# Optimization experiments

Hardware: AMD Instinct MI355X
Metric: run time of the kernel (lower is better)

Reference implementation:

```python
import jax, jax.numpy as jnp
import numpy as np

B = 8
DIM = 256          # __init__ dim; input has 2*DIM channels
H = 32
W = 32
NUM_HEADS = 4
DH_QK = 64         # make_divisible(256*1.0, 8) // 4
DH_V = 64          # dim_out // num_heads
DQK = NUM_HEADS * DH_QK   # 256
DV = NUM_HEADS * DH_V     # 256
SCALE = DH_QK ** -0.5
HIDDEN = 4 * DIM          # mlp_ratio=4 applied to dim
DIM_OUT = DIM
EPS = 1e-5


def setup_inputs() -> dict:
    key = jax.random.key(0)
    ks = jax.random.split(key, 8)
    qkv_out = 2 * DQK + DV   # 768
    return {
        "x": jax.random.normal(ks[0], (B, 2 * DIM, H, W), jnp.float32),
        "qkv_f_w": jax.random.normal(ks[1], (qkv_out, DIM), jnp.float32) * DIM ** -0.5,
        "qkv_p_w": jax.random.normal(ks[2], (qkv_out, DIM), jnp.float32) * DIM ** -0.5,
        "height_rel": jax.random.normal(ks[3], (2 * H - 1, DH_QK), jnp.float32) * SCALE,
        "width_rel": jax.random.normal(ks[4], (2 * W - 1, DH_QK), jnp.float32) * SCALE,
        "ln_gamma": jnp.ones((2 * DV, H, W), jnp.float32),
        "ln_beta": jnp.zeros((2 * DV, H, W), jnp.float32),
        "fc1_w": jax.random.normal(ks[5], (HIDDEN, 2 * DV), jnp.float32) * (2 * DV) ** -0.5,
        "fc1_b": jnp.zeros((HIDDEN,), jnp.float32),
        "fc2_w": jax.random.normal(ks[6], (DIM_OUT, HIDDEN), jnp.float32) * HIDDEN ** -0.5,
        "fc2_b": jnp.zeros((DIM_OUT,), jnp.float32),
    }


def _rel_to_abs(x):
    # x: (b, L, 2L-1) -> (b, L, L) via the pad/reshape shift trick
    b, L, _ = x.shape
    x = jnp.pad(x, ((0, 0), (0, 0), (0, 1)))          # (b, L, 2L)
    xf = x.reshape(b, L * 2 * L)
    xf = jnp.pad(xf, ((0, 0), (0, L - 1)))
    return xf.reshape(b, L + 1, 2 * L - 1)[:, :L, L - 1:]


def _rel_logits_1d(q, rel_k, perm):
    # q: (b, h, w, d); rel_k: (2w-1, d) -> (b, h, w, h, w) after perm
    b, h, w, _ = q.shape
    x = jnp.einsum('bhwd,md->bhwm', q, rel_k).reshape(b * h, w, 2 * w - 1)
    x = _rel_to_abs(x).reshape(b, h, 1, w, w)
    x = jnp.broadcast_to(x, (b, h, h, w, w))
    return x.transpose(perm)


def _pos_embed(q, height_rel, width_rel):
    # q: (B*nh, HW, d) -> relative-position logits (B*nh, HW, HW)
    bh = q.shape[0]
    qs = q.reshape(bh, H, W, DH_QK)
    lw = _rel_logits_1d(qs, width_rel, (0, 1, 3, 2, 4))
    lh = _rel_logits_1d(qs.transpose(0, 2, 1, 3), height_rel, (0, 3, 1, 4, 2))
    return (lh + lw).reshape(bh, H * W, H * W)


def _get_qkv(x, w):
    # 1x1 conv as channel GEMM; x: (B, DIM, H, W)
    qkv = jnp.einsum('bchw,oc->bohw', x, w)
    q, k, v = jnp.split(qkv, [DQK, 2 * DQK], axis=1)
    q = q.reshape(B * NUM_HEADS, DH_QK, H * W).transpose(0, 2, 1)  # (Bh, HW, d)
    k = k.reshape(B * NUM_HEADS, DH_QK, H * W)                      # (Bh, d, HW)
    v = v.reshape(B * NUM_HEADS, DH_V, H * W).transpose(0, 2, 1)    # (Bh, HW, d)
    return q, k, v


def _apply_attn(q, k, v, height_rel, width_rel):
    logits = jnp.einsum('bnd,bdm->bnm', q, k) * SCALE + _pos_embed(q, height_rel, width_rel)
    attn = jax.nn.softmax(logits, axis=-1)
    out = jnp.einsum('bnm,bmd->bnd', attn, v)                       # (Bh, HW, dv)
    return out.transpose(0, 2, 1).reshape(B, DV, H, W)


def reference(x, qkv_f_w, qkv_p_w, height_rel, width_rel, ln_gamma, ln_beta,
              fc1_w, fc1_b, fc2_w, fc2_b):
    x1, x2 = x[:, :DIM], x[:, DIM:]
    qf, kf, vf = _get_qkv(x1, qkv_f_w)
    qp, kp, vp = _get_qkv(x2, qkv_p_w)
    out_f = _apply_attn(qf, kp, vp, height_rel, width_rel)
    out_p = _apply_attn(qp, kf, vf, height_rel, width_rel)
    xpf = jnp.concatenate([out_f, out_p], axis=1)                   # (B, 2*DV, H, W)
    # LayerNorm over normalized_shape = [2*DV, H, W]
    mean = xpf.mean(axis=(1, 2, 3), keepdims=True)
    var = jnp.var(xpf, axis=(1, 2, 3), keepdims=True)
    xpf = (xpf - mean) * jax.lax.rsqrt(var + EPS) * ln_gamma + ln_beta
    # conv-MLP (1x1 convs), exact GELU as torch default
    h = jnp.einsum('bchw,oc->bohw', xpf, fc1_w) + fc1_b[None, :, None, None]
    h = jax.nn.gelu(h, approximate=False)
    out = jnp.einsum('bchw,oc->bohw', h, fc2_w) + fc2_b[None, :, None, None]
    return out  # stride=1 -> pool is identity
```

## Files before the change

kernel.cpp:

```cpp
#include <hip/hip_runtime.h>

#define SCALE 0.125f

typedef short short8 __attribute__((ext_vector_type(8)));
typedef float f32x4 __attribute__((ext_vector_type(4)));
typedef unsigned short us8 __attribute__((ext_vector_type(8)));

typedef __attribute__((address_space(1))) const void gvoid;
typedef __attribute__((address_space(3))) void svoid;
__device__ __forceinline__ void gll16(const void* g, void* l) {
  __builtin_amdgcn_global_load_lds((gvoid*)g, (svoid*)l, 16, 0, 0);
}

__device__ __forceinline__ unsigned short f2bf(float x) {
  unsigned int u = __float_as_uint(x);
  u += 0x7fff + ((u >> 16) & 1);
  return (unsigned short)(u >> 16);
}
__device__ __forceinline__ float bf2f(unsigned short b) {
  return __uint_as_float(((unsigned int)b) << 16);
}
__device__ __forceinline__ float gelu_exact(float x) {
  return 0.5f * x * (1.0f + erff(x * 0.70710678118654752f));
}

__global__ __launch_bounds__(256)
void cast_w(const float* __restrict__ qf, const float* __restrict__ qp,
            const float* __restrict__ f1, const float* __restrict__ f2,
            unsigned short* __restrict__ wc)
{
  const int i4 = (blockIdx.x * 256 + threadIdx.x) * 4;
  const float* src; int off;
  if (i4 < 196608)      { src = qf; off = i4; }
  else if (i4 < 393216) { src = qp; off = i4 - 196608; }
  else if (i4 < 917504) { src = f1; off = i4 - 393216; }
  else                  { src = f2; off = i4 - 917504; }
  const float4 v = *(const float4*)(src + off);
  ushort4 o;
  o.x = f2bf(v.x); o.y = f2bf(v.y); o.z = f2bf(v.z); o.w = f2bf(v.w);
  *(ushort4*)(wc + i4) = o;
}

__global__ __launch_bounds__(256)
void trans_x(const float* __restrict__ x, unsigned short* __restrict__ xT)
{
  __shared__ unsigned short L[64 * 72];
  const int ch0 = blockIdx.x * 64, tok0 = blockIdx.y * 64, z = blockIdx.z;
  const int b = z & 7, path = z >> 3;
  const float* src = x + (size_t)b * 524288 + (size_t)(path * 256 + ch0) * 1024 + tok0;
#pragma unroll
  for (int t = 0; t < 4; ++t) {
    const int i = threadIdx.x + t * 256;
    const int row = i >> 4, c4 = (i & 15) * 4;
    const float4 v = *(const float4*)(src + (size_t)row * 1024 + c4);
    L[(c4 + 0) * 72 + row] = f2bf(v.x);
    L[(c4 + 1) * 72 + row] = f2bf(v.y);
    L[(c4 + 2) * 72 + row] = f2bf(v.z);
    L[(c4 + 3) * 72 + row] = f2bf(v.w);
  }
  __syncthreads();
  unsigned short* dst = xT + (size_t)z * 262144 + (size_t)tok0 * 256 + ch0;
#pragma unroll
  for (int t = 0; t < 2; ++t) {
    const int i = threadIdx.x + t * 256;
    const int row = i >> 3, c8 = (i & 7) * 8;
    *(us8*)(dst + (size_t)row * 256 + c8) = *(const us8*)&L[row * 72 + c8];
  }
}

__global__ __launch_bounds__(256)
void trans_gb(const float* __restrict__ gamma, const float* __restrict__ beta,
              unsigned short* __restrict__ gbT)
{
  __shared__ unsigned short L[64 * 72];
  const int ch0 = blockIdx.x * 64, tok0 = blockIdx.y * 64, which = blockIdx.z;
  const float* src = (which ? beta : gamma) + (size_t)ch0 * 1024 + tok0;
#pragma unroll
  for (int t = 0; t < 4; ++t) {
    const int i = threadIdx.x + t * 256;
    const int row = i >> 4, c4 = (i & 15) * 4;
    const float4 v = *(const float4*)(src + (size_t)row * 1024 + c4);
    L[(c4 + 0) * 72 + row] = f2bf(v.x);
    L[(c4 + 1) * 72 + row] = f2bf(v.y);
    L[(c4 + 2) * 72 + row] = f2bf(v.z);
    L[(c4 + 3) * 72 + row] = f2bf(v.w);
  }
  __syncthreads();
  unsigned short* dst = gbT + (size_t)which * 524288 + (size_t)tok0 * 512 + ch0;
#pragma unroll
  for (int t = 0; t < 2; ++t) {
    const int i = threadIdx.x + t * 256;
    const int row = i >> 3, c8 = (i & 7) * 8;
    *(us8*)(dst + (size_t)row * 512 + c8) = *(const us8*)&L[row * 72 + c8];
  }
}

template<int MODE, int LD, int KLEN>
__global__ __launch_bounds__(256, 3)
void gemm_mf(const unsigned short* __restrict__ A0, const unsigned short* __restrict__ B0,
             unsigned short* __restrict__ qkT, unsigned short* __restrict__ vb,
             unsigned short* __restrict__ hT, float* __restrict__ outF,
             const float* __restrict__ bias)
{
  __shared__ unsigned short As[2][4096];
  __shared__ unsigned short Bs[2][4096];
  const int tid = threadIdx.x;
  const int lane = tid & 63, w = tid >> 6;
  const int c = lane & 15, g = lane >> 4;
  const int wm = w >> 1, wn = w & 1;
  const int m0 = blockIdx.x * 128, n0 = blockIdx.y * 128;
  const int z = blockIdx.z;

  const unsigned short* A;
  const unsigned short* B;
  int zb = z, kc = 0;
  if (MODE == 0) {
    A = A0 + (size_t)(z >> 3) * 196608;
    B = B0 + (size_t)z * 262144;
  } else if (MODE == 1) {
    A = A0;
    B = B0 + (size_t)z * 1024 * LD;
  } else {
    zb = z >> 1; kc = z & 1;
    A = A0 + kc * KLEN;
    B = B0 + (size_t)zb * 1024 * LD + kc * KLEN;
  }

  f32x4 acc[4][4];
#pragma unroll
  for (int mi = 0; mi < 4; ++mi)
#pragma unroll
    for (int ni = 0; ni < 4; ++ni) acc[mi][ni] = (f32x4){0.f, 0.f, 0.f, 0.f};

  const int srow = tid >> 2;
  const int skc8 = (tid & 3) * 8;
  const int sbase = (tid & 192) * 8;

#pragma unroll
  for (int t = 0; t < 2; ++t) {
    gll16(A + (size_t)(m0 + srow + t * 64) * LD + skc8, &As[0][sbase + t * 2048]);
    gll16(B + (size_t)(n0 + srow + t * 64) * LD + skc8, &Bs[0][sbase + t * 2048]);
  }

  const int NK = KLEN / 32;
  for (int ks = 0; ks < NK; ++ks) {
    __syncthreads();
    if (ks + 1 < NK) {
      const int k0 = (ks + 1) * 32;
      const int nb = (ks + 1) & 1;
#pragma unroll
      for (int t = 0; t < 2; ++t) {
        gll16(A + (size_t)(m0 + srow + t * 64) * LD + k0 + skc8, &As[nb][sbase + t * 2048]);
        gll16(B + (size_t)(n0 + srow + t * 64) * LD + k0 + skc8, &Bs[nb][sbase + t * 2048]);
      }
    }
    const unsigned short* Asb = As[ks & 1];
    const unsigned short* Bsb = Bs[ks & 1];
    short8 aF[4], bF[4];
#pragma unroll
    for (int mi = 0; mi < 4; ++mi)
      aF[mi] = *(const short8*)&Asb[(64 * wm + 16 * mi + c) * 32 + g * 8];
#pragma unroll
    for (int ni = 0; ni < 4; ++ni)
      bF[ni] = *(const short8*)&Bsb[(64 * wn + 16 * ni + c) * 32 + g * 8];
#pragma unroll
    for (int mi = 0; mi < 4; ++mi)
#pragma unroll
      for (int ni = 0; ni < 4; ++ni)
        acc[mi][ni] = __builtin_amdgcn_mfma_f32_16x16x32_bf16(aF[mi], bF[ni], acc[mi][ni], 0, 0, 0);
  }

  if (MODE == 0) {
#pragma unroll
    for (int mi = 0; mi < 4; ++mi) {
      const int mb = m0 + 64 * wm + 16 * mi + 4 * g;
#pragma unroll
      for (int ni = 0; ni < 4; ++ni) {
        const int n = n0 + 64 * wn + 16 * ni + c;
        if (mb < 512) {
          ushort4 o4;
          o4.x = f2bf(acc[mi][ni][0]); o4.y = f2bf(acc[mi][ni][1]);
          o4.z = f2bf(acc[mi][ni][2]); o4.w = f2bf(acc[mi][ni][3]);
          *(ushort4*)(qkT + (size_t)z * 524288 + (size_t)n * 512 + mb) = o4;
        } else {
#pragma unroll
          for (int r = 0; r < 4; ++r)
            vb[(size_t)z * 262144 + (size_t)(mb - 512 + r) * 1024 + n] = f2bf(acc[mi][ni][r]);
        }
      }
    }
  } else if (MODE == 1) {
#pragma unroll
    for (int mi = 0; mi < 4; ++mi) {
      const int mb = m0 + 64 * wm + 16 * mi + 4 * g;
      const float4 b4 = *(const float4*)(bias + mb);
#pragma unroll
      for (int ni = 0; ni < 4; ++ni) {
        const int n = n0 + 64 * wn + 16 * ni + c;
        ushort4 o4;
        o4.x = f2bf(gelu_exact(acc[mi][ni][0] + b4.x));
        o4.y = f2bf(gelu_exact(acc[mi][ni][1] + b4.y));
        o4.z = f2bf(gelu_exact(acc[mi][ni][2] + b4.z));
        o4.w = f2bf(gelu_exact(acc[mi][ni][3] + b4.w));
        *(ushort4*)(hT + (size_t)z * 1048576 + (size_t)n * 1024 + mb) = o4;
      }
    }
  } else {
#pragma unroll
    for (int mi = 0; mi < 4; ++mi) {
      const int mb = m0 + 64 * wm + 16 * mi + 4 * g;
      float4 b4 = make_float4(0.f, 0.f, 0.f, 0.f);
      if (kc == 0) b4 = *(const float4*)(bias + mb);
#pragma unroll
      for (int ni = 0; ni < 4; ++ni) {
        const int n = n0 + 64 * wn + 16 * ni + c;
        float* op = outF + (size_t)zb * 262144 + (size_t)mb * 1024 + n;
        atomicAdd(&op[0],    acc[mi][ni][0] + b4.x);
        atomicAdd(&op[1024], acc[mi][ni][1] + b4.y);
        atomicAdd(&op[2048], acc[mi][ni][2] + b4.z);
        atomicAdd(&op[3072], acc[mi][ni][3] + b4.w);
      }
    }
  }
}

__global__ __launch_bounds__(256, 2)
void attn_k(const unsigned short* __restrict__ qkT,
            const unsigned short* __restrict__ vbuf,
            const float* __restrict__ hrel,
            const float* __restrict__ wrel,
            unsigned short* __restrict__ xpfT,
            float* __restrict__ stats)
{
  __shared__ unsigned short Kb[2][4096];
  __shared__ unsigned short Vb[2][4096];
  __shared__ unsigned short Ps[128 * 72];
  __shared__ unsigned short QHt[128 * 34];

  const int tid = threadIdx.x;
  const int lane = tid & 63, w = tid >> 6;
  const int c = lane & 15, g = lane >> 4;
  const int xb = blockIdx.x;
  const int pOut = xb >> 5, bh = xb & 31;
  const int b = bh >> 2, head = bh & 3, pKV = 1 - pOut;
  const int n0 = blockIdx.y * 128;
  const int rb = 32 * w;

  const unsigned short* Qg = qkT + (size_t)(pOut * 8 + b) * 524288 + head * 64;
  const unsigned short* Kg = qkT + (size_t)(pKV * 8 + b) * 524288 + 256 + head * 64;
  const unsigned short* Vg = vbuf + ((size_t)(pKV * 8 + b) * 256 + head * 64) * 1024;

  us8 kr[2], vr[2];
#pragma unroll
  for (int t = 0; t < 2; ++t) {
    const int i = tid + t * 256;
    const int row = i >> 3, ch = i & 7;
    kr[t] = *(const us8*)(Kg + (size_t)row * 512 + ch * 8);
    vr[t] = *(const us8*)(Vg + (size_t)row * 1024 + ch * 8);
  }

  short8 bQ[2][2];
#pragma unroll
  for (int grp = 0; grp < 2; ++grp) {
    const unsigned short* qp = Qg + (size_t)(n0 + rb + 16 * grp + c) * 512 + 8 * g;
    bQ[grp][0] = *(const short8*)(qp);
    bQ[grp][1] = *(const short8*)(qp + 32);
  }

#pragma unroll
  for (int f = 0; f < 4; ++f) {
    const int rr = 16 * f + c;
    const int rrc = rr < 63 ? rr : 62;
    const float sc = rr < 63 ? 1.f : 0.f;
    short8 w0, w1, h0, h1;
#pragma unroll
    for (int j = 0; j < 8; ++j) {
      w0[j] = f2bf(wrel[rrc * 64 + 8 * g + j] * sc);
      w1[j] = f2bf(wrel[rrc * 64 + 32 + 8 * g + j] * sc);
      h0[j] = f2bf(hrel[rrc * 64 + 8 * g + j] * sc);
      h1[j] = f2bf(hrel[rrc * 64 + 32 + 8 * g + j] * sc);
    }
#pragma unroll
    for (int grp = 0; grp < 2; ++grp) {
      f32x4 zw = {0.f, 0.f, 0.f, 0.f};
      zw = __builtin_amdgcn_mfma_f32_16x16x32_bf16(w0, bQ[grp][0], zw, 0, 0, 0);
      zw = __builtin_amdgcn_mfma_f32_16x16x32_bf16(w1, bQ[grp][1], zw, 0, 0, 0);
      f32x4 zh = {0.f, 0.f, 0.f, 0.f};
      zh = __builtin_amdgcn_mfma_f32_16x16x32_bf16(h0, bQ[grp][0], zh, 0, 0, 0);
      zh = __builtin_amdgcn_mfma_f32_16x16x32_bf16(h1, bQ[grp][1], zh, 0, 0, 0);
      const int qrow = rb + 16 * grp + c;
      ushort4 pw;
      pw.x = f2bf(zw[0]); pw.y = f2bf(zw[1]); pw.z = f2bf(zw[2]); pw.w = f2bf(zw[3]);
      *(ushort4*)&Ps[qrow * 72 + 16 * f + 4 * g] = pw;
      const int h1i = (n0 + qrow) >> 5;
#pragma unroll
      for (int r = 0; r < 4; ++r) {
        const int h2 = 16 * f + 4 * g + r - 31 + h1i;
        if (h2 >= 0 && h2 < 32) QHt[qrow * 34 + h2] = f2bf(zh[r]);
      }
    }
  }

  float qwv[2][2][4];
#pragma unroll
  for (int grp = 0; grp < 2; ++grp) {
    const int qrow = rb + 16 * grp + c;
    const int w1i = (n0 + qrow) & 31;
#pragma unroll
    for (int p = 0; p < 2; ++p)
#pragma unroll
      for (int r = 0; r < 4; ++r)
        qwv[grp][p][r] = bf2f(Ps[qrow * 72 + (16 * p + 4 * g + r - w1i + 31)]);
  }

#pragma unroll
  for (int t = 0; t < 2; ++t) {
    const int i = tid + t * 256;
    const int row = i >> 3, ch = i & 7;
    const int p = row * 64 + ((ch ^ (row & 7)) * 8);
    *(us8*)&Kb[0][p] = kr[t];
    *(us8*)&Vb[0][p] = vr[t];
  }

  float lsum[2] = {0.f, 0.f};
  f32x4 O[2][4];
#pragma unroll
  for (int grp = 0; grp < 2; ++grp)
#pragma unroll
    for (int f = 0; f < 4; ++f) O[grp][f] = (f32x4){0.f, 0.f, 0.f, 0.f};

  for (int mt = 0; mt < 16; ++mt) {
    __syncthreads();
    if (mt < 15) {
      const int m0n = (mt + 1) * 64;
#pragma unroll
      for (int t = 0; t < 2; ++t) {
        const int i = tid + t * 256;
        const int row = i >> 3, ch = i & 7;
        kr[t] = *(const us8*)(Kg + (size_t)(m0n + row) * 512 + ch * 8);
        vr[t] = *(const us8*)(Vg + (size_t)row * 1024 + m0n + ch * 8);
      }
    }
    const unsigned short* Ks = Kb[mt & 1];
    const unsigned short* Vs = Vb[mt & 1];

    short8 kA[4][2];
#pragma unroll
    for (int f = 0; f < 4; ++f) {
      const int row = 16 * f + c;
      kA[f][0] = *(const short8*)&Ks[row * 64 + ((g ^ (row & 7)) * 8)];
      kA[f][1] = *(const short8*)&Ks[row * 64 + (((4 + g) ^ (row & 7)) * 8)];
    }
#pragma unroll
    for (int grp = 0; grp < 2; ++grp) {
      const int qrow = rb + 16 * grp + c;
      const float qh0 = bf2f(QHt[qrow * 34 + 2 * mt]);
      const float qh1 = bf2f(QHt[qrow * 34 + 2 * mt + 1]);
#pragma unroll
      for (int f = 0; f < 4; ++f) {
        f32x4 z = {0.f, 0.f, 0.f, 0.f};
        z = __builtin_amdgcn_mfma_f32_16x16x32_bf16(kA[f][0], bQ[grp][0], z, 0, 0, 0);
        z = __builtin_amdgcn_mfma_f32_16x16x32_bf16(kA[f][1], bQ[grp][1], z, 0, 0, 0);
        const float qh = (f >= 2) ? qh1 : qh0;
        const float* qwp = qwv[grp][f & 1];
        const float p0 = __expf(fmaf(z[0], SCALE, qh + qwp[0]));
        const float p1 = __expf(fmaf(z[1], SCALE, qh + qwp[1]));
        const float p2 = __expf(fmaf(z[2], SCALE, qh + qwp[2]));
        const float p3 = __expf(fmaf(z[3], SCALE, qh + qwp[3]));
        lsum[grp] += (p0 + p1) + (p2 + p3);
        ushort4 pk;
        pk.x = f2bf(p0); pk.y = f2bf(p1); pk.z = f2bf(p2); pk.w = f2bf(p3);
        *(ushort4*)&Ps[qrow * 72 + 16 * f + 4 * g] = pk;
      }
    }
    short8 vB[4][2];
#pragma unroll
    for (int f = 0; f < 4; ++f) {
      const int row = 16 * f + c;
      vB[f][0] = *(const short8*)&Vs[row * 64 + ((g ^ (row & 7)) * 8)];
      vB[f][1] = *(const short8*)&Vs[row * 64 + (((4 + g) ^ (row & 7)) * 8)];
    }
#pragma unroll
    for (int grp = 0; grp < 2; ++grp) {
      const int qrow = rb + 16 * grp + c;
      const short8 aP0 = *(const short8*)&Ps[qrow * 72 + 8 * g];
      const short8 aP1 = *(const short8*)&Ps[qrow * 72 + 32 + 8 * g];
#pragma unroll
      for (int f = 0; f < 4; ++f) {
        O[grp][f] = __builtin_amdgcn_mfma_f32_16x16x32_bf16(aP0, vB[f][0], O[grp][f], 0, 0, 0);
        O[grp][f] = __builtin_amdgcn_mfma_f32_16x16x32_bf16(aP1, vB[f][1], O[grp][f], 0, 0, 0);
      }
    }
    if (mt < 15) {
#pragma unroll
      for (int t = 0; t < 2; ++t) {
        const int i = tid + t * 256;
        const int row = i >> 3, ch = i & 7;
        const int p = row * 64 + ((ch ^ (row & 7)) * 8);
        *(us8*)&Kb[(mt + 1) & 1][p] = kr[t];
        *(us8*)&Vb[(mt + 1) & 1][p] = vr[t];
      }
    }
  }

#pragma unroll
  for (int grp = 0; grp < 2; ++grp) {
    lsum[grp] += __shfl_xor(lsum[grp], 16);
    lsum[grp] += __shfl_xor(lsum[grp], 32);
  }
  float linv[2][4];
#pragma unroll
  for (int grp = 0; grp < 2; ++grp)
#pragma unroll
    for (int r = 0; r < 4; ++r)
      linv[grp][r] = 1.0f / __shfl(lsum[grp], 4 * g + r);

  float ssum = 0.f, ssq = 0.f;
#pragma unroll
  for (int grp = 0; grp < 2; ++grp)
#pragma unroll
    for (int f = 0; f < 4; ++f)
#pragma unroll
      for (int r = 0; r < 4; ++r) {
        const float v = O[grp][f][r] * linv[grp][r];
        ssum += v;
        ssq = fmaf(v, v, ssq);
        Ps[(rb + 16 * grp + 4 * g + r) * 72 + 16 * f + c] = f2bf(v);
      }
#pragma unroll
  for (int off = 1; off < 64; off <<= 1) {
    ssum += __shfl_xor(ssum, off);
    ssq  += __shfl_xor(ssq, off);
  }
  if (lane == 0) {
    atomicAdd(&stats[b * 2 + 0], ssum);
    atomicAdd(&stats[b * 2 + 1], ssq);
  }

  __syncthreads();
  unsigned short* dst = xpfT + ((size_t)b * 1024 + n0) * 512 + pOut * 256 + head * 64;
#pragma unroll
  for (int t = 0; t < 4; ++t) {
    const int i = tid + t * 256;
    const int row = i >> 3, ch = i & 7;
    *(us8*)(dst + (size_t)row * 512 + ch * 8) = *(const us8*)&Ps[row * 72 + ch * 8];
  }
}

__global__ __launch_bounds__(256)
void ln_k(const unsigned short* __restrict__ xpfT, const unsigned short* __restrict__ gbT,
          const float* __restrict__ stats, unsigned short* __restrict__ xln)
{
  const int i = blockIdx.x * 256 + threadIdx.x;
  const int b = i >> 16, off = i & 65535;
  const float invN = 1.0f / 524288.0f;
  const float mean = stats[b * 2] * invN;
  const float var = stats[b * 2 + 1] * invN - mean * mean;
  const float rstd = rsqrtf(var + 1e-5f);
  const us8 xv = *(const us8*)(xpfT + (size_t)i * 8);
  const us8 gv = *(const us8*)(gbT + (size_t)off * 8);
  const us8 bv = *(const us8*)(gbT + 524288 + (size_t)off * 8);
  us8 ov;
#pragma unroll
  for (int j = 0; j < 8; ++j)
    ov[j] = f2bf((bf2f(xv[j]) - mean) * rstd * bf2f(gv[j]) + bf2f(bv[j]));
  *(us8*)(xln + (size_t)i * 8) = ov;
}

extern "C" void kernel_launch(void* const* d_in, const int* in_sizes, int n_in,
                              void* d_out, int out_size, void* d_ws, size_t ws_size,
                              hipStream_t stream)
{
  const float* x     = (const float*)d_in[0];
  const float* qkvfw = (const float*)d_in[1];
  const float* qkvpw = (const float*)d_in[2];
  const float* hrel  = (const float*)d_in[3];
  const float* wrel  = (const float*)d_in[4];
  const float* gamma = (const float*)d_in[5];
  const float* beta  = (const float*)d_in[6];
  const float* fc1w  = (const float*)d_in[7];
  const float* fc1b  = (const float*)d_in[8];
  const float* fc2w  = (const float*)d_in[9];
  const float* fc2b  = (const float*)d_in[10];
  float* out = (float*)d_out;

  float* stats = (float*)d_ws;
  unsigned short* wc   = (unsigned short*)(stats + 64);
  unsigned short* xT   = wc + 1179648;
  unsigned short* gbT  = xT + 4194304;
  unsigned short* qkT  = gbT + 1048576;
  unsigned short* vbuf = qkT + 8388608;
  unsigned short* xpfT = vbuf + 4194304;
  unsigned short* hT   = xpfT + 4194304;

  hipMemsetAsync(stats, 0, 64 * sizeof(float), stream);
  hipMemsetAsync(out, 0, (size_t)out_size * sizeof(float), stream);

  cast_w<<<1152, 256, 0, stream>>>(qkvfw, qkvpw, fc1w, fc2w, wc);
  trans_x<<<dim3(4, 16, 16), 256, 0, stream>>>(x, xT);
  trans_gb<<<dim3(8, 16, 2), 256, 0, stream>>>(gamma, beta, gbT);

  gemm_mf<0, 256, 256><<<dim3(6, 8, 16), 256, 0, stream>>>(
      wc, xT, qkT, vbuf, nullptr, nullptr, nullptr);

  attn_k<<<dim3(64, 8), 256, 0, stream>>>(qkT, vbuf, hrel, wrel, xpfT, stats);

  ln_k<<<2048, 256, 0, stream>>>(xpfT, gbT, stats, xT);

  gemm_mf<1, 512, 512><<<dim3(8, 8, 8), 256, 0, stream>>>(
      wc + 393216, xT, nullptr, nullptr, hT, nullptr, fc1b);

  gemm_mf<3, 1024, 512><<<dim3(2, 8, 16), 256, 0, stream>>>(
      wc + 917504, hT, nullptr, nullptr, nullptr, out, fc2b);
}
```

Baseline: 249.5 us.

## Fuse prep kernels, swizzle GEMM LDS layout, split fc2 K four ways

Merges the weight cast, x transpose and gamma/beta transpose into a single launch, and zeroes the stats buffer inside it so the stats memset is no longer needed. The GEMM LDS tiles now use an XOR-swizzled layout for the global-to-LDS loads and fragment reads, which is meant to cut bank conflicts. The fc2 GEMM splits K into four chunks instead of two, doubling its grid at the cost of more atomic adds into the output. In the attention loop the barrier moves after the next-tile global loads so those loads are issued before the wait.

```diff
diff --git a/kernel.cpp b/kernel.cpp
--- a/kernel.cpp
+++ b/kernel.cpp
@@ -25,32 +25,50 @@
 }
 
 __global__ __launch_bounds__(256)
-void cast_w(const float* __restrict__ qf, const float* __restrict__ qp,
+void prep_k(const float* __restrict__ qf, const float* __restrict__ qp,
             const float* __restrict__ f1, const float* __restrict__ f2,
-            unsigned short* __restrict__ wc)
-{
-  const int i4 = (blockIdx.x * 256 + threadIdx.x) * 4;
-  const float* src; int off;
-  if (i4 < 196608)      { src = qf; off = i4; }
-  else if (i4 < 393216) { src = qp; off = i4 - 196608; }
-  else if (i4 < 917504) { src = f1; off = i4 - 393216; }
-  else                  { src = f2; off = i4 - 917504; }
-  const float4 v = *(const float4*)(src + off);
-  ushort4 o;
-  o.x = f2bf(v.x); o.y = f2bf(v.y); o.z = f2bf(v.z); o.w = f2bf(v.w);
-  *(ushort4*)(wc + i4) = o;
-}
-
-__global__ __launch_bounds__(256)
-void trans_x(const float* __restrict__ x, unsigned short* __restrict__ xT)
+            const float* __restrict__ x, const float* __restrict__ gamma,
+            const float* __restrict__ beta, unsigned short* __restrict__ wc,
+            unsigned short* __restrict__ xT, unsigned short* __restrict__ gbT,
+            float* __restrict__ stats)
 {
   __shared__ unsigned short L[64 * 72];
-  const int ch0 = blockIdx.x * 64, tok0 = blockIdx.y * 64, z = blockIdx.z;
-  const int b = z & 7, path = z >> 3;
-  const float* src = x + (size_t)b * 524288 + (size_t)(path * 256 + ch0) * 1024 + tok0;
+  const int bx = blockIdx.x;
+  const int tid = threadIdx.x;
+  if (bx < 1152) {
+    if (bx == 0 && tid < 64) stats[tid] = 0.f;
+    const int i4 = (bx * 256 + tid) * 4;
+    const float* src; int off;
+    if (i4 < 196608)      { src = qf; off = i4; }
+    else if (i4 < 393216) { src = qp; off = i4 - 196608; }
+    else if (i4 < 917504) { src = f1; off = i4 - 393216; }
+    else                  { src = f2; off = i4 - 917504; }
+    const float4 v = *(const float4*)(src + off);
+    ushort4 o;
+    o.x = f2bf(v.x); o.y = f2bf(v.y); o.z = f2bf(v.z); o.w = f2bf(v.w);
+    *(ushort4*)(wc + i4) = o;
+    return;
+  }
+  const float* src;
+  unsigned short* dst;
+  int dstride;
+  if (bx < 2176) {
+    const int t = bx - 1152;
+    const int ch0 = (t & 3) * 64, tok0 = ((t >> 2) & 15) * 64, z = t >> 6;
+    const int b = z & 7, path = z >> 3;
+    src = x + (size_t)b * 524288 + (size_t)(path * 256 + ch0) * 1024 + tok0;
+    dst = xT + (size_t)z * 262144 + (size_t)tok0 * 256 + ch0;
+    dstride = 256;
+  } else {
+    const int u = bx - 2176;
+    const int ch0 = (u & 7) * 64, tok0 = ((u >> 3) & 15) * 64, which = u >> 7;
+    src = (which ? beta : gamma) + (size_t)ch0 * 1024 + tok0;
+    dst = gbT + (size_t)which * 524288 + (size_t)tok0 * 512 + ch0;
+    dstride = 512;
+  }
 #pragma unroll
   for (int t = 0; t < 4; ++t) {
-    const int i = threadIdx.x + t * 256;
+    const int i = tid + t * 256;
     const int row = i >> 4, c4 = (i & 15) * 4;
     const float4 v = *(const float4*)(src + (size_t)row * 1024 + c4);
     L[(c4 + 0) * 72 + row] = f2bf(v.x);
@@ -59,39 +77,11 @@
     L[(c4 + 3) * 72 + row] = f2bf(v.w);
   }
   __syncthreads();
-  unsigned short* dst = xT + (size_t)z * 262144 + (size_t)tok0 * 256 + ch0;
 #pragma unroll
   for (int t = 0; t < 2; ++t) {
-    const int i = threadIdx.x + t * 256;
+    const int i = tid + t * 256;
     const int row = i >> 3, c8 = (i & 7) * 8;
-    *(us8*)(dst + (size_t)row * 256 + c8) = *(const us8*)&L[row * 72 + c8];
-  }
-}
-
-__global__ __launch_bounds__(256)
-void trans_gb(const float* __restrict__ gamma, const float* __restrict__ beta,
-              unsigned short* __restrict__ gbT)
-{
-  __shared__ unsigned short L[64 * 72];
-  const int ch0 = blockIdx.x * 64, tok0 = blockIdx.y * 64, which = blockIdx.z;
-  const float* src = (which ? beta : gamma) + (size_t)ch0 * 1024 + tok0;
-#pragma unroll
-  for (int t = 0; t < 4; ++t) {
-    const int i = threadIdx.x + t * 256;
-    const int row = i >> 4, c4 = (i & 15) * 4;
-    const float4 v = *(const float4*)(src + (size_t)row * 1024 + c4);
-    L[(c4 + 0) * 72 + row] = f2bf(v.x);
-    L[(c4 + 1) * 72 + row] = f2bf(v.y);
-    L[(c4 + 2) * 72 + row] = f2bf(v.z);
-    L[(c4 + 3) * 72 + row] = f2bf(v.w);
-  }
-  __syncthreads();
-  unsigned short* dst = gbT + (size_t)which * 524288 + (size_t)tok0 * 512 + ch0;
-#pragma unroll
-  for (int t = 0; t < 2; ++t) {
-    const int i = threadIdx.x + t * 256;
-    const int row = i >> 3, c8 = (i & 7) * 8;
-    *(us8*)(dst + (size_t)row * 512 + c8) = *(const us8*)&L[row * 72 + c8];
+    *(us8*)(dst + (size_t)row * dstride + c8) = *(const us8*)&L[row * 72 + c8];
   }
 }
 
@@ -121,7 +111,7 @@
     A = A0;
     B = B0 + (size_t)z * 1024 * LD;
   } else {
-    zb = z >> 1; kc = z & 1;
+    zb = z >> 2; kc = z & 3;
     A = A0 + kc * KLEN;
     B = B0 + (size_t)zb * 1024 * LD + kc * KLEN;
   }
@@ -132,14 +122,21 @@
 #pragma unroll
     for (int ni = 0; ni < 4; ++ni) acc[mi][ni] = (f32x4){0.f, 0.f, 0.f, 0.f};
 
-  const int srow = tid >> 2;
-  const int skc8 = (tid & 3) * 8;
+  int grow[2], gkc8[2];
+#pragma unroll
+  for (int t = 0; t < 2; ++t) {
+    const int i = tid + t * 256;
+    const int sp = i >> 3;
+    const int ls = (i & 7) ^ (sp & 7);
+    grow[t] = sp * 2 + (ls >> 2);
+    gkc8[t] = (ls & 3) * 8;
+  }
   const int sbase = (tid & 192) * 8;
 
 #pragma unroll
   for (int t = 0; t < 2; ++t) {
-    gll16(A + (size_t)(m0 + srow + t * 64) * LD + skc8, &As[0][sbase + t * 2048]);
-    gll16(B + (size_t)(n0 + srow + t * 64) * LD + skc8, &Bs[0][sbase + t * 2048]);
+    gll16(A + (size_t)(m0 + grow[t]) * LD + gkc8[t], &As[0][sbase + t * 2048]);
+    gll16(B + (size_t)(n0 + grow[t]) * LD + gkc8[t], &Bs[0][sbase + t * 2048]);
   }
 
   const int NK = KLEN / 32;
@@ -150,19 +147,25 @@
       const int nb = (ks + 1) & 1;
 #pragma unroll
       for (int t = 0; t < 2; ++t) {
-        gll16(A + (size_t)(m0 + srow + t * 64) * LD + k0 + skc8, &As[nb][sbase + t * 2048]);
-        gll16(B + (size_t)(n0 + srow + t * 64) * LD + k0 + skc8, &Bs[nb][sbase + t * 2048]);
+        gll16(A + (size_t)(m0 + grow[t]) * LD + k0 + gkc8[t], &As[nb][sbase + t * 2048]);
+        gll16(B + (size_t)(n0 + grow[t]) * LD + k0 + gkc8[t], &Bs[nb][sbase + t * 2048]);
       }
     }
     const unsigned short* Asb = As[ks & 1];
     const unsigned short* Bsb = Bs[ks & 1];
     short8 aF[4], bF[4];
 #pragma unroll
-    for (int mi = 0; mi < 4; ++mi)
-      aF[mi] = *(const short8*)&Asb[(64 * wm + 16 * mi + c) * 32 + g * 8];
-#pragma unroll
-    for (int ni = 0; ni < 4; ++ni)
-      bF[ni] = *(const short8*)&Bsb[(64 * wn + 16 * ni + c) * 32 + g * 8];
+    for (int mi = 0; mi < 4; ++mi) {
+      const int row = 64 * wm + 16 * mi + c;
+      const int rp = row >> 1;
+      aF[mi] = *(const short8*)&Asb[rp * 64 + ((((row & 1) * 4 + g) ^ (rp & 7)) * 8)];
+    }
+#pragma unroll
+    for (int ni = 0; ni < 4; ++ni) {
+      const int row = 64 * wn + 16 * ni + c;
+      const int rp = row >> 1;
+      bF[ni] = *(const short8*)&Bsb[rp * 64 + ((((row & 1) * 4 + g) ^ (rp & 7)) * 8)];
+    }
 #pragma unroll
     for (int mi = 0; mi < 4; ++mi)
 #pragma unroll
@@ -330,7 +333,6 @@
     for (int f = 0; f < 4; ++f) O[grp][f] = (f32x4){0.f, 0.f, 0.f, 0.f};
 
   for (int mt = 0; mt < 16; ++mt) {
-    __syncthreads();
     if (mt < 15) {
       const int m0n = (mt + 1) * 64;
 #pragma unroll
@@ -341,6 +343,7 @@
         vr[t] = *(const us8*)(Vg + (size_t)row * 1024 + m0n + ch * 8);
       }
     }
+    __syncthreads();
     const unsigned short* Ks = Kb[mt & 1];
     const unsigned short* Vs = Vb[mt & 1];
 
@@ -493,12 +496,10 @@
   unsigned short* xpfT = vbuf + 4194304;
   unsigned short* hT   = xpfT + 4194304;
 
-  hipMemsetAsync(stats, 0, 64 * sizeof(float), stream);
   hipMemsetAsync(out, 0, (size_t)out_size * sizeof(float), stream);
 
-  cast_w<<<1152, 256, 0, stream>>>(qkvfw, qkvpw, fc1w, fc2w, wc);
-  trans_x<<<dim3(4, 16, 16), 256, 0, stream>>>(x, xT);
-  trans_gb<<<dim3(8, 16, 2), 256, 0, stream>>>(gamma, beta, gbT);
+  prep_k<<<2432, 256, 0, stream>>>(qkvfw, qkvpw, fc1w, fc2w, x, gamma, beta,
+                                   wc, xT, gbT, stats);
 
   gemm_mf<0, 256, 256><<<dim3(6, 8, 16), 256, 0, stream>>>(
       wc, xT, qkT, vbuf, nullptr, nullptr, nullptr);
@@ -510,6 +511,6 @@
   gemm_mf<1, 512, 512><<<dim3(8, 8, 8), 256, 0, stream>>>(
       wc + 393216, xT, nullptr, nullptr, hT, nullptr, fc1b);
 
-  gemm_mf<3, 1024, 512><<<dim3(2, 8, 16), 256, 0, stream>>>(
+  gemm_mf<3, 1024, 256><<<dim3(2, 8, 32), 256, 0, stream>>>(
       wc + 917504, hT, nullptr, nullptr, nullptr, out, fc2b);
 }
```

New measurement: 252.7 us. No clear change (+1.3%).
